# Kernel tuning notes

Measured on AMD Instinct MI355X. Metric: run time of the kernel, lower is better.

The kernel has to match this reference:

```python
import jax, jax.numpy as jnp
import numpy as np

CAPACITY_FACTOR = 1.25
AUX_W = 0.1
Z_W = 0.001


def setup_inputs() -> dict:
    key = jax.random.key(0)
    k0, k1, k2, k3 = jax.random.split(key, 4)
    B, T, C, E, H = 4, 2048, 896, 3, 3584
    x = jax.random.normal(k0, (B, T, C), dtype=jnp.float32)
    Wr = jax.random.normal(k1, (E, C), dtype=jnp.float32) * 0.02   # router Linear(C->E)
    W1 = jax.random.normal(k2, (E, H, C), dtype=jnp.float32) * 0.02  # per-expert Linear(C->H)
    W2 = jax.random.normal(k3, (E, C, H), dtype=jnp.float32) * 0.02  # per-expert Linear(H->C)
    return {"x": x, "Wr": Wr, "W1": W1, "W2": W2}


def reference(x, Wr, W1, W2):
    B, T, C = x.shape
    E = Wr.shape[0]
    N = B * T
    capacity = int(CAPACITY_FACTOR * N / E)  # static

    # --- router ---
    logits = jnp.einsum('btc,ec->bte', x, Wr)                      # [B,T,E]
    z_loss = Z_W * jnp.mean(jax.nn.logsumexp(logits, axis=-1) ** 2)
    probs = jax.nn.softmax(logits, axis=-1)
    pf = probs.reshape(N, E)
    expert_index = jnp.argmax(pf, axis=-1)                          # top-1
    mask = jax.nn.one_hot(expert_index, E, dtype=x.dtype)           # [N,E]

    # capacity-limited dispatch: per expert keep top-`capacity` tokens by router prob.
    # (When an expert has <= capacity tokens this keeps all of them, matching the
    #  torch reference's two branches.)
    scores = jnp.where(mask > 0, pf, -jnp.inf).T                    # [E,N]
    _, top_idx = jax.lax.top_k(scores, capacity)                    # [E,capacity]
    disp = jnp.zeros((E, N), dtype=x.dtype).at[jnp.arange(E)[:, None], top_idx].set(1.0)
    dispatch = (disp * mask.T).T                                    # [N,E], kills -inf picks

    gates = pf * dispatch
    gates = gates / (jnp.sum(gates, axis=-1, keepdims=True) + 1e-6)  # [N,E]

    aux_loss = AUX_W * jnp.sum(dispatch.mean(axis=0) * pf.mean(axis=0)) * E

    # --- experts (dense over tokens, gated combine; dropout in eval = identity) ---
    xf = x.reshape(N, C)
    h = jax.nn.gelu(jnp.einsum('nc,ehc->neh', xf, W1), approximate=False)  # [N,E,H]
    y = jnp.einsum('neh,ech->nec', h, W2)                                   # [N,E,C]
    out = xf + jnp.einsum('nec,ne->nc', y, gates)                           # residual + combine
    return out.reshape(B, T, C), aux_loss + z_loss
```

## Files before the change

kernel.cpp:

```cpp
#include <hip/hip_runtime.h>
#include <stdint.h>

#define B_ 4
#define T_ 2048
#define C_ 896
#define E_ 3
#define H_ 3584
#define N_ 8192
#define CVB 512

typedef __attribute__((ext_vector_type(8))) short short8;
typedef __attribute__((ext_vector_type(4))) float f32x4;

#define OFF_XB   ((size_t)0)
#define OFF_W1B  ((size_t)14680064)
#define OFF_W2B  ((size_t)33947648)
#define OFF_HB   ((size_t)53215232)
#define OFF_PERM ((size_t)111935488)
#define OFF_EID  ((size_t)112033792)
#define OFF_GATE ((size_t)112066560)
#define OFF_PBUF ((size_t)112099328)
#define OFF_LSE2 ((size_t)112197632)
#define OFF_CNT  ((size_t)112230400)
#define OFF_P    OFF_XB

static __device__ __forceinline__ unsigned short f2b(float f) {
  union { float f; unsigned u; } v; v.f = f;
  unsigned r = v.u + 0x7FFFu + ((v.u >> 16) & 1u);
  return (unsigned short)(r >> 16);
}

static __device__ __forceinline__ float gelu_fast(float v) {
  float u = 0.7978845608f * v * fmaf(0.044715f * v, v, 1.0f);
  u = fminf(u, 20.0f);
  float t = __expf(2.0f * u);
  return v * t * __builtin_amdgcn_rcpf(t + 1.0f);
}

static __device__ __forceinline__ int xcd_chunk(int lin, int total) {
  int q = total >> 3, r = total & 7;
  int xcd = lin & 7, idx = lin >> 3;
  return (xcd < r ? xcd * (q + 1) : r * (q + 1) + (xcd - r) * q) + idx;
}

static __device__ __forceinline__ void grp_decode(int t, int rt, int ncol, int RG, int CG,
                                                  int* rowt, int* colt) {
  const int fullbands = rt / RG;
  const int bandsz = RG * ncol;
  if (t < fullbands * bandsz) {
    int band = t / bandsz, tr = t % bandsz;
    int cg = tr / (CG * RG), r2 = tr % (CG * RG);
    *rowt = band * RG + r2 / CG;
    *colt = cg * CG + r2 % CG;
  } else {
    int t2 = t - fullbands * bandsz;
    int tail = rt - fullbands * RG;
    int cg = t2 / (CG * tail), r2 = t2 % (CG * tail);
    *rowt = fullbands * RG + r2 / CG;
    *colt = cg * CG + r2 % CG;
  }
}

static __device__ __forceinline__ void cvt_stride(const float* __restrict__ src,
                                                  unsigned short* __restrict__ dst,
                                                  int n4, int bid, int nblk) {
  const int stride = nblk * 256;
  for (int i = bid * 256 + threadIdx.x; i < n4; i += stride) {
    float4 v = reinterpret_cast<const float4*>(src)[i];
    ushort4 o;
    o.x = f2b(v.x); o.y = f2b(v.y); o.z = f2b(v.z); o.w = f2b(v.w);
    reinterpret_cast<ushort4*>(dst)[i] = o;
  }
}

__global__ __launch_bounds__(256) void router_kernel(
    const float* __restrict__ x, const float* __restrict__ Wr,
    unsigned short* __restrict__ xb,
    int* __restrict__ eid, float* __restrict__ gate,
    float* __restrict__ pbuf, float* __restrict__ lse2,
    const float* __restrict__ W1, unsigned short* __restrict__ w1b) {
  if (blockIdx.x >= N_ / 8) {
    cvt_stride(W1, w1b, E_ * H_ * C_ / 4, blockIdx.x - N_ / 8, 1024);
    return;
  }
  const int tid = threadIdx.x;
  const int sub = tid & 31;
  const int n = blockIdx.x * 8 + (tid >> 5);
  const float4* xr = reinterpret_cast<const float4*>(x + (size_t)n * C_);
  ushort4* xw = reinterpret_cast<ushort4*>(xb + (size_t)n * C_);
  const float4* w0p = reinterpret_cast<const float4*>(Wr + 0 * C_);
  const float4* w1p = reinterpret_cast<const float4*>(Wr + 1 * C_);
  const float4* w2p = reinterpret_cast<const float4*>(Wr + 2 * C_);
  float s0 = 0.f, s1 = 0.f, s2 = 0.f;
#pragma unroll
  for (int j = 0; j < 7; ++j) {
    const int idx = sub + 32 * j;
    float4 v = xr[idx];
    ushort4 o;
    o.x = f2b(v.x); o.y = f2b(v.y); o.z = f2b(v.z); o.w = f2b(v.w);
    xw[idx] = o;
    float4 a = w0p[idx], b = w1p[idx], c = w2p[idx];
    s0 += v.x * a.x + v.y * a.y + v.z * a.z + v.w * a.w;
    s1 += v.x * b.x + v.y * b.y + v.z * b.z + v.w * b.w;
    s2 += v.x * c.x + v.y * c.y + v.z * c.z + v.w * c.w;
  }
#pragma unroll
  for (int off = 16; off > 0; off >>= 1) {
    s0 += __shfl_xor(s0, off);
    s1 += __shfl_xor(s1, off);
    s2 += __shfl_xor(s2, off);
  }
  if (sub == 0) {
    float m = fmaxf(s0, fmaxf(s1, s2));
    float e0 = expf(s0 - m), e1 = expf(s1 - m), e2 = expf(s2 - m);
    float sum = e0 + e1 + e2;
    float p0 = e0 / sum, p1 = e1 / sum, p2 = e2 / sum;
    int am = 0; float best = s0;
    if (s1 > best) { best = s1; am = 1; }
    if (s2 > best) { best = s2; am = 2; }
    float pa = (am == 0) ? p0 : ((am == 1) ? p1 : p2);
    eid[n] = am;
    gate[n] = pa / (pa + 1e-6f);
    pbuf[n * 3 + 0] = p0; pbuf[n * 3 + 1] = p1; pbuf[n * 3 + 2] = p2;
    float lse = m + logf(sum);
    lse2[n] = lse * lse;
  }
}

__global__ __launch_bounds__(1024) void scatter_kernel(const int* __restrict__ eid,
                                                       int* __restrict__ counts,
                                                       int* __restrict__ perm) {
  __shared__ int hist[E_];
  __shared__ int base[E_];
  const int t = threadIdx.x;
  const int n = blockIdx.x * 1024 + t;
  if (t < E_) hist[t] = 0;
  __syncthreads();
  int e = eid[n];
  int l = atomicAdd(&hist[e], 1);
  __syncthreads();
  if (t < E_) base[t] = atomicAdd(&counts[t], hist[t]);
  __syncthreads();
  perm[e * N_ + base[e] + l] = n;
}

#define STAGE_TILE(bufA, bufB)                                                          \
  do {                                                                                  \
    _Pragma("unroll")                                                                   \
    for (int i_ = 0; i_ < 4; ++i_) {                                                    \
      __builtin_amdgcn_global_load_lds(                                                 \
          (const __attribute__((address_space(1))) void*)pA_[i_],                       \
          (__attribute__((address_space(3))) void*)&(bufA)[(wv * 4 + i_) * 512], 16, 0, 0); \
    }                                                                                   \
    _Pragma("unroll")                                                                   \
    for (int i_ = 0; i_ < 4; ++i_) {                                                    \
      __builtin_amdgcn_global_load_lds(                                                 \
          (const __attribute__((address_space(1))) void*)pB_[i_],                       \
          (__attribute__((address_space(3))) void*)&(bufB)[(wv * 4 + i_) * 512], 16, 0, 0); \
    }                                                                                   \
    _Pragma("unroll")                                                                   \
    for (int i_ = 0; i_ < 4; ++i_) { pA_[i_] += 64; pB_[i_] += 64; }                    \
  } while (0)

#define COMPUTE_TILE(bufA, bufB)                                                        \
  do {                                                                                  \
    _Pragma("unroll")                                                                   \
    for (int kk = 0; kk < 2; ++kk) {                                                    \
      const int sl_ = ((kk * 4 + (lane >> 4)) ^ (lane & 7)) * 8;                        \
      short8 af[4], bfv[4];                                                             \
      _Pragma("unroll")                                                                 \
      for (int m = 0; m < 4; ++m) {                                                     \
        int row = wm * 64 + m * 16 + (lane & 15);                                       \
        af[m] = *reinterpret_cast<const short8*>(&(bufA)[row * 64 + sl_]);              \
      }                                                                                 \
      _Pragma("unroll")                                                                 \
      for (int nn = 0; nn < 4; ++nn) {                                                  \
        int row = wn * 64 + nn * 16 + (lane & 15);                                      \
        bfv[nn] = *reinterpret_cast<const short8*>(&(bufB)[row * 64 + sl_]);            \
      }                                                                                 \
      _Pragma("unroll")                                                                 \
      for (int m = 0; m < 4; ++m)                                                       \
        _Pragma("unroll")                                                               \
        for (int nn = 0; nn < 4; ++nn)                                                  \
          acc[m][nn] = __builtin_amdgcn_mfma_f32_16x16x32_bf16(af[m], bfv[nn], acc[m][nn], 0, 0, 0); \
    }                                                                                   \
  } while (0)

#define K_LOOP(NT)                                                                      \
  do {                                                                                  \
    for (int kt = 0; kt < (NT); ++kt) {                                                 \
      STAGE_TILE(shA, shB);                                                             \
      __syncthreads();                                                                  \
      COMPUTE_TILE(shA, shB);                                                           \
      __syncthreads();                                                                  \
    }                                                                                   \
  } while (0)

__global__ __launch_bounds__(256) void gemm1_kernel(
    const unsigned short* __restrict__ xb,
    const unsigned short* __restrict__ w1b,
    unsigned short* __restrict__ h,
    const int* __restrict__ perm, const int* __restrict__ counts,
    const float* __restrict__ W2, unsigned short* __restrict__ w2b) {
  if (blockIdx.x < CVB) {
    cvt_stride(W2, w2b, E_ * C_ * H_ / 4, blockIdx.x, CVB);
    return;
  }
  const int c0 = counts[0], c1 = counts[1], c2 = counts[2];
  const int rt0 = (c0 + 127) >> 7, rt1 = (c1 + 127) >> 7, rt2 = (c2 + 127) >> 7;
  const int n0 = rt0 * 28, n1 = rt1 * 28, n2 = rt2 * 28;
  const int total = n0 + n1 + n2;
  const int lin = blockIdx.x - CVB;
  if (lin >= total) return;
  const int wgid = xcd_chunk(lin, total);
  int e, rem, rt_e, count;
  if (wgid < n0)            { e = 0; rem = wgid;           rt_e = rt0; count = c0; }
  else if (wgid < n0 + n1)  { e = 1; rem = wgid - n0;      rt_e = rt1; count = c1; }
  else                      { e = 2; rem = wgid - n0 - n1; rt_e = rt2; count = c2; }
  int rowt, colt;
  grp_decode(rem, rt_e, 28, 8, 7, &rowt, &colt);
  const int row0 = rowt * 128;
  const int col0 = colt * 128;
  const int tid = threadIdx.x, lane = tid & 63, wv = tid >> 6;
  const int wm = wv >> 1, wn = wv & 1;
  const int* permE = perm + e * N_;
  const unsigned short* w1e = w1b + (size_t)e * H_ * C_;

  __shared__ __align__(16) unsigned short shA[128 * 64];
  __shared__ __align__(16) unsigned short shB[128 * 64];

  f32x4 acc[4][4];
#pragma unroll
  for (int i = 0; i < 4; ++i)
#pragma unroll
    for (int j = 0; j < 4; ++j) acc[i][j] = (f32x4){0.f, 0.f, 0.f, 0.f};

  const int cc = (((lane & 7) ^ (lane >> 3))) * 8;
  const unsigned short* pA_[4];
  const unsigned short* pB_[4];
#pragma unroll
  for (int i = 0; i < 4; ++i) {
    int s = row0 + (wv * 4 + i) * 8 + (lane >> 3);
    if (s >= count) s = count - 1;
    pA_[i] = xb + (size_t)permE[s] * C_ + cc;
    int r = (wv * 4 + i) * 8 + (lane >> 3);
    pB_[i] = w1e + (size_t)(col0 + r) * C_ + cc;
  }

  K_LOOP(C_ / 64);

#pragma unroll
  for (int m = 0; m < 4; ++m) {
    int rbase = wm * 64 + m * 16 + (lane >> 4) * 4;
#pragma unroll
    for (int i = 0; i < 4; ++i) {
      int s = row0 + rbase + i;
      if (s < count) {
        int ntok = permE[s];
#pragma unroll
        for (int nn = 0; nn < 4; ++nn) {
          int col = col0 + wn * 64 + nn * 16 + (lane & 15);
          h[(size_t)ntok * H_ + col] = f2b(gelu_fast(acc[m][nn][i]));
        }
      }
    }
  }
}

__global__ __launch_bounds__(256) void gemm2_kernel(
    const unsigned short* __restrict__ h,
    const unsigned short* __restrict__ w2b,
    const float* __restrict__ x,
    const float* __restrict__ gate,
    float* __restrict__ out, float* __restrict__ P,
    const int* __restrict__ perm, const int* __restrict__ counts) {
  const int c0 = counts[0], c1 = counts[1], c2 = counts[2];
  const int rt0 = (c0 + 127) >> 7, rt1 = (c1 + 127) >> 7, rt2 = (c2 + 127) >> 7;
  const int n0 = rt0 * 14, n1 = rt1 * 14, n2 = rt2 * 14;
  const int total = n0 + n1 + n2;
  const int lin = blockIdx.x;
  if (lin >= total) return;
  const int wgid = xcd_chunk(lin, total);
  int e, rem, rt_e, count;
  if (wgid < n0)            { e = 0; rem = wgid;           rt_e = rt0; count = c0; }
  else if (wgid < n0 + n1)  { e = 1; rem = wgid - n0;      rt_e = rt1; count = c1; }
  else                      { e = 2; rem = wgid - n0 - n1; rt_e = rt2; count = c2; }
  int rowt, c14;
  grp_decode(rem, rt_e, 14, 4, 7, &rowt, &c14);
  const int ks = c14 / 7;
  const int colt = c14 % 7;
  const int row0 = rowt * 128;
  const int col0 = colt * 128;
  const int kbase = ks * (H_ / 2);
  const int tid = threadIdx.x, lane = tid & 63, wv = tid >> 6;
  const int wm = wv >> 1, wn = wv & 1;
  const int* permE = perm + e * N_;
  const unsigned short* w2e = w2b + (size_t)e * C_ * H_;

  __shared__ __align__(16) unsigned short shA[128 * 64];
  __shared__ __align__(16) unsigned short shB[128 * 64];

  f32x4 acc[4][4];
#pragma unroll
  for (int i = 0; i < 4; ++i)
#pragma unroll
    for (int j = 0; j < 4; ++j) acc[i][j] = (f32x4){0.f, 0.f, 0.f, 0.f};

  const int cc = (((lane & 7) ^ (lane >> 3))) * 8;
  const unsigned short* pA_[4];
  const unsigned short* pB_[4];
#pragma unroll
  for (int i = 0; i < 4; ++i) {
    int s = row0 + (wv * 4 + i) * 8 + (lane >> 3);
    if (s >= count) s = count - 1;
    pA_[i] = h + (size_t)permE[s] * H_ + kbase + cc;
    int r = (wv * 4 + i) * 8 + (lane >> 3);
    pB_[i] = w2e + (size_t)(col0 + r) * H_ + kbase + cc;
  }

  K_LOOP((H_ / 2) / 64);

#pragma unroll
  for (int m = 0; m < 4; ++m) {
    int rbase = wm * 64 + m * 16 + (lane >> 4) * 4;
#pragma unroll
    for (int i = 0; i < 4; ++i) {
      int s = row0 + rbase + i;
      if (s < count) {
        int ntok = permE[s];
        float g = gate[ntok];
        if (ks == 0) {
#pragma unroll
          for (int nn = 0; nn < 4; ++nn) {
            int col = col0 + wn * 64 + nn * 16 + (lane & 15);
            out[(size_t)ntok * C_ + col] = x[(size_t)ntok * C_ + col] + g * acc[m][nn][i];
          }
        } else {
#pragma unroll
          for (int nn = 0; nn < 4; ++nn) {
            int col = col0 + wn * 64 + nn * 16 + (lane & 15);
            P[(size_t)ntok * C_ + col] = g * acc[m][nn][i];
          }
        }
      }
    }
  }
}

__global__ __launch_bounds__(256) void combine_kernel(
    float* __restrict__ out, const float* __restrict__ P, int n4,
    const float* __restrict__ lse2, const float* __restrict__ pbuf,
    const int* __restrict__ eid) {
  int stride = gridDim.x * blockDim.x;
  for (int i = blockIdx.x * blockDim.x + threadIdx.x; i < n4; i += stride) {
    float4 a = reinterpret_cast<float4*>(out)[i];
    float4 b = reinterpret_cast<const float4*>(P)[i];
    a.x += b.x; a.y += b.y; a.z += b.z; a.w += b.w;
    reinterpret_cast<float4*>(out)[i] = a;
  }
  if (blockIdx.x == 0) {
    __shared__ float sh[7][256];
    float a = 0.f, p0 = 0.f, p1 = 0.f, p2 = 0.f, c0 = 0.f, c1 = 0.f, c2 = 0.f;
    for (int n = threadIdx.x; n < N_; n += 256) {
      a += lse2[n];
      p0 += pbuf[n * 3 + 0]; p1 += pbuf[n * 3 + 1]; p2 += pbuf[n * 3 + 2];
      int e = eid[n];
      c0 += (e == 0); c1 += (e == 1); c2 += (e == 2);
    }
    sh[0][threadIdx.x] = a;
    sh[1][threadIdx.x] = p0; sh[2][threadIdx.x] = p1; sh[3][threadIdx.x] = p2;
    sh[4][threadIdx.x] = c0; sh[5][threadIdx.x] = c1; sh[6][threadIdx.x] = c2;
    for (int s = 128; s > 0; s >>= 1) {
      __syncthreads();
      if (threadIdx.x < (unsigned)s)
#pragma unroll
        for (int q = 0; q < 7; ++q) sh[q][threadIdx.x] += sh[q][threadIdx.x + s];
    }
    if (threadIdx.x == 0) {
      const float invN = 1.0f / (float)N_;
      float z = 0.001f * (sh[0][0] * invN);
      float aux = 0.1f * (float)E_ *
                  (sh[4][0] * invN * sh[1][0] * invN +
                   sh[5][0] * invN * sh[2][0] * invN +
                   sh[6][0] * invN * sh[3][0] * invN);
      out[(size_t)N_ * C_] = z + aux;
    }
  }
}

extern "C" void kernel_launch(void* const* d_in, const int* in_sizes, int n_in,
                              void* d_out, int out_size, void* d_ws, size_t ws_size,
                              hipStream_t stream) {
  const float* x  = (const float*)d_in[0];
  const float* Wr = (const float*)d_in[1];
  const float* W1 = (const float*)d_in[2];
  const float* W2 = (const float*)d_in[3];
  float* out = (float*)d_out;
  char* ws = (char*)d_ws;

  unsigned short* xb  = (unsigned short*)(ws + OFF_XB);
  unsigned short* w1b = (unsigned short*)(ws + OFF_W1B);
  unsigned short* w2b = (unsigned short*)(ws + OFF_W2B);
  unsigned short* hb  = (unsigned short*)(ws + OFF_HB);
  int*   perm  = (int*)(ws + OFF_PERM);
  int*   eid   = (int*)(ws + OFF_EID);
  float* gate  = (float*)(ws + OFF_GATE);
  float* pbuf  = (float*)(ws + OFF_PBUF);
  float* lse2  = (float*)(ws + OFF_LSE2);
  int*   counts = (int*)(ws + OFF_CNT);
  float* P     = (float*)(ws + OFF_P);

  hipMemsetAsync(counts, 0, E_ * sizeof(int), stream);

  router_kernel<<<2048, 256, 0, stream>>>(x, Wr, xb, eid, gate, pbuf, lse2, W1, w1b);
  scatter_kernel<<<N_ / 1024, 1024, 0, stream>>>(eid, counts, perm);

  gemm1_kernel<<<CVB + 27 * 28 * E_, 256, 0, stream>>>(xb, w1b, hb, perm, counts, W2, w2b);
  gemm2_kernel<<<27 * 14 * E_, 256, 0, stream>>>(hb, w2b, x, gate, out, P, perm, counts);
  combine_kernel<<<2048, 256, 0, stream>>>(out, P, N_ * C_ / 4, lse2, pbuf, eid);
}
```

Before: 216.7 us.

## Enlarge GEMM row tiles to 256 with 512-thread workgroups

Both expert GEMMs now use 256x128 output tiles computed by 8 waves per 512-thread workgroup instead of 128x128 tiles with 4 waves. Each wave now loads 4 A rows-chunks and 2 B chunks, so the weight tile in LDS is shared across more token rows. This lowers global weight traffic per output and reduces grid size (also halving conversion blocks). It raises LDS use per block and may leave CUs with fewer blocks, plus more row-padding waste for the last tile per expert.

```diff
diff --git a/kernel.cpp b/kernel.cpp
--- a/kernel.cpp
+++ b/kernel.cpp
@@ -7,7 +7,8 @@
 #define E_ 3
 #define H_ 3584
 #define N_ 8192
-#define CVB 512
+#define CVB 256
+#define NRT 14
 
 typedef __attribute__((ext_vector_type(8))) short short8;
 typedef __attribute__((ext_vector_type(4))) float f32x4;
@@ -64,8 +65,8 @@
 static __device__ __forceinline__ void cvt_stride(const float* __restrict__ src,
                                                   unsigned short* __restrict__ dst,
                                                   int n4, int bid, int nblk) {
-  const int stride = nblk * 256;
-  for (int i = bid * 256 + threadIdx.x; i < n4; i += stride) {
+  const int stride = nblk * blockDim.x;
+  for (int i = bid * blockDim.x + threadIdx.x; i < n4; i += stride) {
     float4 v = reinterpret_cast<const float4*>(src)[i];
     ushort4 o;
     o.x = f2b(v.x); o.y = f2b(v.y); o.z = f2b(v.z); o.w = f2b(v.w);
@@ -144,25 +145,27 @@
   perm[e * N_ + base[e] + l] = n;
 }
 
-#define STAGE_TILE(bufA, bufB)                                                          \
+#define STAGE_TILE()                                                                    \
   do {                                                                                  \
     _Pragma("unroll")                                                                   \
     for (int i_ = 0; i_ < 4; ++i_) {                                                    \
       __builtin_amdgcn_global_load_lds(                                                 \
           (const __attribute__((address_space(1))) void*)pA_[i_],                       \
-          (__attribute__((address_space(3))) void*)&(bufA)[(wv * 4 + i_) * 512], 16, 0, 0); \
+          (__attribute__((address_space(3))) void*)&shA[(wv * 4 + i_) * 512], 16, 0, 0); \
     }                                                                                   \
     _Pragma("unroll")                                                                   \
-    for (int i_ = 0; i_ < 4; ++i_) {                                                    \
+    for (int i_ = 0; i_ < 2; ++i_) {                                                    \
       __builtin_amdgcn_global_load_lds(                                                 \
           (const __attribute__((address_space(1))) void*)pB_[i_],                       \
-          (__attribute__((address_space(3))) void*)&(bufB)[(wv * 4 + i_) * 512], 16, 0, 0); \
+          (__attribute__((address_space(3))) void*)&shB[(wv * 2 + i_) * 512], 16, 0, 0); \
     }                                                                                   \
     _Pragma("unroll")                                                                   \
-    for (int i_ = 0; i_ < 4; ++i_) { pA_[i_] += 64; pB_[i_] += 64; }                    \
+    for (int i_ = 0; i_ < 4; ++i_) { pA_[i_] += 64; }                                   \
+    _Pragma("unroll")                                                                   \
+    for (int i_ = 0; i_ < 2; ++i_) { pB_[i_] += 64; }                                   \
   } while (0)
 
-#define COMPUTE_TILE(bufA, bufB)                                                        \
+#define COMPUTE_TILE()                                                                  \
   do {                                                                                  \
     _Pragma("unroll")                                                                   \
     for (int kk = 0; kk < 2; ++kk) {                                                    \
@@ -171,12 +174,12 @@
       _Pragma("unroll")                                                                 \
       for (int m = 0; m < 4; ++m) {                                                     \
         int row = wm * 64 + m * 16 + (lane & 15);                                       \
-        af[m] = *reinterpret_cast<const short8*>(&(bufA)[row * 64 + sl_]);              \
+        af[m] = *reinterpret_cast<const short8*>(&shA[row * 64 + sl_]);                 \
       }                                                                                 \
       _Pragma("unroll")                                                                 \
       for (int nn = 0; nn < 4; ++nn) {                                                  \
         int row = wn * 64 + nn * 16 + (lane & 15);                                      \
-        bfv[nn] = *reinterpret_cast<const short8*>(&(bufB)[row * 64 + sl_]);            \
+        bfv[nn] = *reinterpret_cast<const short8*>(&shB[row * 64 + sl_]);               \
       }                                                                                 \
       _Pragma("unroll")                                                                 \
       for (int m = 0; m < 4; ++m)                                                       \
@@ -189,14 +192,14 @@
 #define K_LOOP(NT)                                                                      \
   do {                                                                                  \
     for (int kt = 0; kt < (NT); ++kt) {                                                 \
-      STAGE_TILE(shA, shB);                                                             \
+      STAGE_TILE();                                                                     \
       __syncthreads();                                                                  \
-      COMPUTE_TILE(shA, shB);                                                           \
+      COMPUTE_TILE();                                                                   \
       __syncthreads();                                                                  \
     }                                                                                   \
   } while (0)
 
-__global__ __launch_bounds__(256) void gemm1_kernel(
+__global__ __launch_bounds__(512) void gemm1_kernel(
     const unsigned short* __restrict__ xb,
     const unsigned short* __restrict__ w1b,
     unsigned short* __restrict__ h,
@@ -207,7 +210,7 @@
     return;
   }
   const int c0 = counts[0], c1 = counts[1], c2 = counts[2];
-  const int rt0 = (c0 + 127) >> 7, rt1 = (c1 + 127) >> 7, rt2 = (c2 + 127) >> 7;
+  const int rt0 = (c0 + 255) >> 8, rt1 = (c1 + 255) >> 8, rt2 = (c2 + 255) >> 8;
   const int n0 = rt0 * 28, n1 = rt1 * 28, n2 = rt2 * 28;
   const int total = n0 + n1 + n2;
   const int lin = blockIdx.x - CVB;
@@ -218,15 +221,15 @@
   else if (wgid < n0 + n1)  { e = 1; rem = wgid - n0;      rt_e = rt1; count = c1; }
   else                      { e = 2; rem = wgid - n0 - n1; rt_e = rt2; count = c2; }
   int rowt, colt;
-  grp_decode(rem, rt_e, 28, 8, 7, &rowt, &colt);
-  const int row0 = rowt * 128;
+  grp_decode(rem, rt_e, 28, 4, 7, &rowt, &colt);
+  const int row0 = rowt * 256;
   const int col0 = colt * 128;
   const int tid = threadIdx.x, lane = tid & 63, wv = tid >> 6;
   const int wm = wv >> 1, wn = wv & 1;
   const int* permE = perm + e * N_;
   const unsigned short* w1e = w1b + (size_t)e * H_ * C_;
 
-  __shared__ __align__(16) unsigned short shA[128 * 64];
+  __shared__ __align__(16) unsigned short shA[256 * 64];
   __shared__ __align__(16) unsigned short shB[128 * 64];
 
   f32x4 acc[4][4];
@@ -237,13 +240,16 @@
 
   const int cc = (((lane & 7) ^ (lane >> 3))) * 8;
   const unsigned short* pA_[4];
-  const unsigned short* pB_[4];
+  const unsigned short* pB_[2];
 #pragma unroll
   for (int i = 0; i < 4; ++i) {
-    int s = row0 + (wv * 4 + i) * 8 + (lane >> 3);
+    int s = row0 + wv * 32 + i * 8 + (lane >> 3);
     if (s >= count) s = count - 1;
     pA_[i] = xb + (size_t)permE[s] * C_ + cc;
-    int r = (wv * 4 + i) * 8 + (lane >> 3);
+  }
+#pragma unroll
+  for (int i = 0; i < 2; ++i) {
+    int r = wv * 16 + i * 8 + (lane >> 3);
     pB_[i] = w1e + (size_t)(col0 + r) * C_ + cc;
   }
 
@@ -267,7 +273,7 @@
   }
 }
 
-__global__ __launch_bounds__(256) void gemm2_kernel(
+__global__ __launch_bounds__(512) void gemm2_kernel(
     const unsigned short* __restrict__ h,
     const unsigned short* __restrict__ w2b,
     const float* __restrict__ x,
@@ -275,7 +281,7 @@
     float* __restrict__ out, float* __restrict__ P,
     const int* __restrict__ perm, const int* __restrict__ counts) {
   const int c0 = counts[0], c1 = counts[1], c2 = counts[2];
-  const int rt0 = (c0 + 127) >> 7, rt1 = (c1 + 127) >> 7, rt2 = (c2 + 127) >> 7;
+  const int rt0 = (c0 + 255) >> 8, rt1 = (c1 + 255) >> 8, rt2 = (c2 + 255) >> 8;
   const int n0 = rt0 * 14, n1 = rt1 * 14, n2 = rt2 * 14;
   const int total = n0 + n1 + n2;
   const int lin = blockIdx.x;
@@ -286,10 +292,10 @@
   else if (wgid < n0 + n1)  { e = 1; rem = wgid - n0;      rt_e = rt1; count = c1; }
   else                      { e = 2; rem = wgid - n0 - n1; rt_e = rt2; count = c2; }
   int rowt, c14;
-  grp_decode(rem, rt_e, 14, 4, 7, &rowt, &c14);
+  grp_decode(rem, rt_e, 14, 2, 7, &rowt, &c14);
   const int ks = c14 / 7;
   const int colt = c14 % 7;
-  const int row0 = rowt * 128;
+  const int row0 = rowt * 256;
   const int col0 = colt * 128;
   const int kbase = ks * (H_ / 2);
   const int tid = threadIdx.x, lane = tid & 63, wv = tid >> 6;
@@ -297,7 +303,7 @@
   const int* permE = perm + e * N_;
   const unsigned short* w2e = w2b + (size_t)e * C_ * H_;
 
-  __shared__ __align__(16) unsigned short shA[128 * 64];
+  __shared__ __align__(16) unsigned short shA[256 * 64];
   __shared__ __align__(16) unsigned short shB[128 * 64];
 
   f32x4 acc[4][4];
@@ -308,13 +314,16 @@
 
   const int cc = (((lane & 7) ^ (lane >> 3))) * 8;
   const unsigned short* pA_[4];
-  const unsigned short* pB_[4];
+  const unsigned short* pB_[2];
 #pragma unroll
   for (int i = 0; i < 4; ++i) {
-    int s = row0 + (wv * 4 + i) * 8 + (lane >> 3);
+    int s = row0 + wv * 32 + i * 8 + (lane >> 3);
     if (s >= count) s = count - 1;
     pA_[i] = h + (size_t)permE[s] * H_ + kbase + cc;
-    int r = (wv * 4 + i) * 8 + (lane >> 3);
+  }
+#pragma unroll
+  for (int i = 0; i < 2; ++i) {
+    int r = wv * 16 + i * 8 + (lane >> 3);
     pB_[i] = w2e + (size_t)(col0 + r) * H_ + kbase + cc;
   }
 
@@ -415,7 +424,7 @@
   router_kernel<<<2048, 256, 0, stream>>>(x, Wr, xb, eid, gate, pbuf, lse2, W1, w1b);
   scatter_kernel<<<N_ / 1024, 1024, 0, stream>>>(eid, counts, perm);
 
-  gemm1_kernel<<<CVB + 27 * 28 * E_, 256, 0, stream>>>(xb, w1b, hb, perm, counts, W2, w2b);
-  gemm2_kernel<<<27 * 14 * E_, 256, 0, stream>>>(hb, w2b, x, gate, out, P, perm, counts);
+  gemm1_kernel<<<CVB + NRT * 28 * E_, 512, 0, stream>>>(xb, w1b, hb, perm, counts, W2, w2b);
+  gemm2_kernel<<<NRT * 14 * E_, 512, 0, stream>>>(hb, w2b, x, gate, out, P, perm, counts);
   combine_kernel<<<2048, 256, 0, stream>>>(out, P, N_ * C_ / 4, lse2, pbuf, eid);
 }
```

Result: faster. 181.5 us (-16.2%).
